# Optimization experiments

Hardware: AMD Instinct MI355X
Metric: run time of the kernel (lower is better)

## Reference

```python
import jax, jax.numpy as jnp
import numpy as np

SPIKING_T = 8        # args['spiking_t']
V_TH = 1.0           # spikingjelly IFNode default v_threshold
TAU = 2.0            # NonSpikingLIFNode tau
ALPHA = 4.0          # spikingjelly default Sigmoid surrogate alpha
MIN_LOG_STD, MAX_LOG_STD = -20.0, 2.0
LOG_2PI = float(np.log(2.0 * np.pi))

@jax.custom_vjp
def spike(x):
    # Heaviside forward (spikingjelly surrogate.Sigmoid behavior)
    return (x >= 0.0).astype(x.dtype)

def _spike_fwd(x):
    return spike(x), x

def _spike_bwd(x, g):
    s = jax.nn.sigmoid(ALPHA * x)
    return (g * ALPHA * s * (1.0 - s),)

spike.defvjp(_spike_fwd, _spike_bwd)


def setup_inputs() -> dict:
    key = jax.random.key(0)
    ks = jax.random.split(key, 8)
    B, N, H, A = 8192, 128, 1024, 32
    def lin_w(k, fan_in, fan_out):
        return jax.random.normal(k, (fan_in, fan_out), dtype=jnp.float32) / jnp.sqrt(float(fan_in))
    return {
        "state": jax.random.normal(ks[0], (B, N), dtype=jnp.float32),
        "w1": lin_w(ks[1], N, H),
        "b1": jnp.full((H,), 1e-6, dtype=jnp.float32),
        "w2": lin_w(ks[2], H, H),
        "b2": jnp.full((H,), 1e-6, dtype=jnp.float32),
        "w3": lin_w(ks[3], H, 2 * A),
        "b3": jnp.full((2 * A,), 1e-6, dtype=jnp.float32),
        "eps": jax.random.normal(ks[4], (B, A), dtype=jnp.float32),
    }


def reference(state, w1, b1, w2, b2, w3, b3, eps):
    B = state.shape[0]
    H = w1.shape[1]
    O = w3.shape[1]
    v1 = jnp.zeros((B, H), state.dtype)
    v2 = jnp.zeros((B, H), state.dtype)
    v3 = jnp.zeros((B, O), state.dtype)

    def step(carry, _):
        v1, v2, v3 = carry
        # IF node 1: charge, fire, hard reset to 0
        h1 = v1 + state @ w1 + b1
        s1 = spike(h1 - V_TH)
        v1 = h1 * (1.0 - s1)
        # IF node 2
        h2 = v2 + s1 @ w2 + b2
        s2 = spike(h2 - V_TH)
        v2 = h2 * (1.0 - s2)
        # NonSpiking LIF (decay_input=True, v_reset=0): v += (x - v)/tau
        x3 = s2 @ w3 + b3
        v3 = v3 + (x3 - v3) / TAU
        return (v1, v2, v3), None

    (v1, v2, v3), _ = jax.lax.scan(step, (v1, v2, v3), None, length=SPIKING_T)

    mu, log_std = jnp.split(v3, 2, axis=-1)
    log_std = jnp.clip(log_std, MIN_LOG_STD, MAX_LOG_STD)
    std = jnp.exp(log_std)
    z = mu + std * eps            # Normal rsample
    action = jnp.tanh(z)
    # Normal(mu, std).log_prob(z) = -eps^2/2 - log_std - 0.5*log(2*pi)
    log_prob = (-0.5 * eps * eps - log_std - 0.5 * LOG_2PI) \
               - jnp.log(1.0 - action * action + 1e-7)
    log_prob = jnp.sum(log_prob, axis=-1, keepdims=True)
    return action, log_prob
```

## Files before the change

kernel.cpp:

```cpp
#include <hip/hip_runtime.h>

typedef float    f32x4 __attribute__((ext_vector_type(4)));
typedef int      i32x4 __attribute__((ext_vector_type(4)));
typedef unsigned u32x4 __attribute__((ext_vector_type(4)));

typedef const __attribute__((address_space(1))) void* gptr_t;
typedef __attribute__((address_space(3))) void* lptr_t;

__device__ __forceinline__ void gload_lds16(const void* g, void* l) {
  __builtin_amdgcn_global_load_lds((gptr_t)g, (lptr_t)l, 16, 0, 0);
}

constexpr int Bsz  = 8192;
constexpr int Nin  = 128;
constexpr int Hd   = 1024;
constexpr int Aact = 32;
constexpr int Od   = 64;
constexpr int KC = 384;
constexpr float DELTA = 1.5e-4f;
constexpr unsigned WCAP = 262144;

constexpr float CSCALE = 1.1920928955078125e-7f;

__global__ __launch_bounds__(256)
void prep_kernel(const float* __restrict__ state, const float* __restrict__ w1,
                 const float* __restrict__ b1,
                 const float* __restrict__ w2, const float* __restrict__ w3,
                 unsigned char* __restrict__ s1pack,
                 char* __restrict__ p1, char* __restrict__ p2, char* __restrict__ p3,
                 char* __restrict__ r1, char* __restrict__ r2, char* __restrict__ r3,
                 float* __restrict__ w2tf, unsigned* __restrict__ wcnt) {
  __shared__ float sAT[64][68];
  __shared__ float sB[64][68];
  const int tid = threadIdx.x;

  if (blockIdx.x >= 2048) {
    if (blockIdx.x == 2048 && tid < 8) wcnt[tid] = 0;
    const int u = (blockIdx.x - 2048) * 4 + (tid >> 6);
    const int lane = tid & 63;
    const int l15 = lane & 15, quad = lane >> 4;
    const int pn = u >> 4;
    const int kb = u & 15;
    const bool isw3 = (pn >= Hd / 16);
    const int pnl = isw3 ? pn - Hd / 16 : pn;
    const float* src = isw3 ? w3 : w2;
    const int N = isw3 ? Od : Hd;
    const int n = pnl * 16 + l15;
    const int k0 = kb * 64 + quad * 16;
    char* d1 = isw3 ? r1 : p1;
    char* d2 = isw3 ? r2 : p2;
    char* d3 = isw3 ? r3 : p3;
    float wv[16];
    char o1[16], o2[16], o3[16];
#pragma unroll
    for (int e = 0; e < 16; ++e) {
      float w = src[(size_t)(k0 + e) * N + n];
      wv[e] = w;
      float m1 = rintf(w * 512.0f);
      float q1 = w - m1 * (1.0f / 512.0f);
      float m2 = rintf(q1 * 65536.0f);
      float q2 = q1 - m2 * (1.0f / 65536.0f);
      float m3 = rintf(q2 * 8388608.0f);
      o1[e] = (char)(int)m1; o2[e] = (char)(int)m2; o3[e] = (char)(int)m3;
    }
    size_t off = ((size_t)pnl * 16 + kb) * 1024 + (size_t)lane * 16;
#pragma unroll
    for (int e = 0; e < 16; ++e) {
      d1[off + e] = o1[e]; d2[off + e] = o2[e]; d3[off + e] = o3[e];
    }
    if (!isw3) {
#pragma unroll
      for (int e = 0; e < 16; ++e)
        w2tf[(size_t)n * Hd + k0 + e] = wv[e];
    }
    return;
  }

  const int m0 = (blockIdx.x & 127) * 64, n0 = (blockIdx.x >> 7) * 64;
  const int tx = tid & 15, ty = tid >> 4;
  float acc[4][4] = {};
#pragma unroll
  for (int h = 0; h < 2; ++h) {
    if (h) __syncthreads();
    for (int idx = tid; idx < 1024; idx += 256) {
      int r = idx >> 4, c4 = (idx & 15) << 2;
      float4 v = *(const float4*)(state + (size_t)(m0 + r) * Nin + h * 64 + c4);
      int pc = (r + c4) & 63;
      sAT[c4 + 0][pc] = v.x; sAT[c4 + 1][pc] = v.y;
      sAT[c4 + 2][pc] = v.z; sAT[c4 + 3][pc] = v.w;
    }
    for (int idx = tid; idx < 1024; idx += 256) {
      int r = idx >> 4, c4 = (idx & 15) << 2;
      *(float4*)&sB[r][c4] = *(const float4*)(w1 + (size_t)(h * 64 + r) * Hd + n0 + c4);
    }
    __syncthreads();
    for (int k = 0; k < 64; ++k) {
      int cb = ((ty << 2) + (k & ~3)) & 63;
      float4 a4 = *(const float4*)&sAT[k][cb];
      float4 b = *(const float4*)&sB[k][tx * 4];
      float a[4] = {a4.x, a4.y, a4.z, a4.w};
#pragma unroll
      for (int i = 0; i < 4; ++i) {
        acc[i][0] = __fmaf_rn(a[i], b.x, acc[i][0]);
        acc[i][1] = __fmaf_rn(a[i], b.y, acc[i][1]);
        acc[i][2] = __fmaf_rn(a[i], b.z, acc[i][2]);
        acc[i][3] = __fmaf_rn(a[i], b.w, acc[i][3]);
      }
    }
  }
#pragma unroll
  for (int i = 0; i < 4; ++i) {
    int m = m0 + ty * 4 + i;
    unsigned pack = 0;
#pragma unroll
    for (int j = 0; j < 4; ++j) {
      int n = n0 + tx * 4 + j;
      float x = acc[i][j];
      float bb = b1[n];
      float v = 0.0f;
      unsigned bits = 0;
#pragma unroll
      for (int t = 0; t < 8; ++t) {
        float h2 = __fadd_rn(__fadd_rn(v, x), bb);
        if (h2 >= 1.0f) { bits |= (1u << t); v = 0.0f; } else { v = h2; }
      }
      pack |= bits << (8 * j);
    }
    *(unsigned*)(s1pack + (size_t)m * Hd + n0 + tx * 4) = pack;
  }
}

__global__ __launch_bounds__(256, 3)
void gemm2i8_kernel(const unsigned char* __restrict__ s1pack,
                    const char* __restrict__ q1, const char* __restrict__ q2,
                    const char* __restrict__ q3,
                    const float* __restrict__ b2,
                    unsigned char* __restrict__ s2p,
                    unsigned* __restrict__ wcnt, unsigned* __restrict__ wlist) {
  constexpr int NKB = Hd / 64;
  __shared__ __align__(16) unsigned char lA[3][64 * 64];
  __shared__ __align__(16) char lB[3][3072];
  const int tid = threadIdx.x;
  const int m0 = blockIdx.x * 64;
  const int n0 = blockIdx.y * 16;
  const int wave = tid >> 6, lane = tid & 63, l15 = lane & 15, quad = lane >> 4;
  const char* bplane = (wave == 0) ? q1 : (wave == 1) ? q2 : q3;
  const unsigned char* asrc = s1pack
      + (size_t)(m0 + ((tid >> 6) << 4) + (tid & 15)) * Hd + ((tid >> 4) & 3) * 16;
  const char* bsrc2 = bplane + (size_t)blockIdx.y * NKB * 1024 + (size_t)lane * 16;
  i32x4 acc[3][8] = {};

  auto stage = [&](int kb, int buf) {
    gload_lds16(asrc + kb * 64, &lA[buf][tid * 16]);
    if (wave < 3)
      gload_lds16(bsrc2 + (size_t)kb * 1024, &lB[buf][wave * 1024 + lane * 16]);
  };
  stage(0, 0); stage(1, 1);

#pragma unroll
  for (int kb = 0; kb < NKB; ++kb) {
    const int cur = kb % 3;
    if (kb < NKB - 1) {
      if (wave < 3) asm volatile("s_waitcnt vmcnt(2)" ::: "memory");
      else          asm volatile("s_waitcnt vmcnt(1)" ::: "memory");
    } else {
      asm volatile("s_waitcnt vmcnt(0)" ::: "memory");
    }
    __builtin_amdgcn_s_barrier();
    asm volatile("" ::: "memory");
    u32x4 ad = *(const u32x4*)&lA[cur][wave * 1024 + lane * 16];
    i32x4 fb0 = *(const i32x4*)&lB[cur][lane * 16];
    i32x4 fb1 = *(const i32x4*)&lB[cur][1024 + lane * 16];
    i32x4 fb2 = *(const i32x4*)&lB[cur][2048 + lane * 16];
    if (kb + 2 < NKB) stage(kb + 2, (kb + 2) % 3);
#pragma unroll
    for (int t = 0; t < 8; ++t) {
      const unsigned msk = 0x01010101u << t;
      i32x4 af;
      af[0] = (int)(ad[0] & msk);
      af[1] = (int)(ad[1] & msk);
      af[2] = (int)(ad[2] & msk);
      af[3] = (int)(ad[3] & msk);
      acc[0][t] = __builtin_amdgcn_mfma_i32_16x16x64_i8(af, fb0, acc[0][t], 0, 0, 0);
      acc[1][t] = __builtin_amdgcn_mfma_i32_16x16x64_i8(af, fb1, acc[1][t], 0, 0, 0);
      acc[2][t] = __builtin_amdgcn_mfma_i32_16x16x64_i8(af, fb2, acc[2][t], 0, 0, 0);
    }
  }
  const int n = n0 + l15;
  const float bb = b2[n];
#pragma unroll
  for (int r = 0; r < 4; ++r) {
    int m = m0 + wave * 16 + quad * 4 + r;
    size_t idx = (size_t)m * Hd + n;
    float v = 0.0f;
    unsigned bits = 0;
#pragma unroll
    for (int t = 0; t < 8; ++t) {
      int a0 = acc[0][t][r] >> t;
      int a1 = acc[1][t][r] >> t;
      int a2 = acc[2][t][r] >> t;
      int s = (a0 << 14) + (a1 << 7) + a2;
      float G = (float)s * ((t == 7) ? -CSCALE : CSCALE);
      float h = __fadd_rn(__fadd_rn(v, G), bb);
      if (__builtin_expect(__builtin_fabsf(h - 1.0f) < DELTA, 0)) {
        unsigned pos = atomicAdd(wcnt, 1u);
        if (pos < WCAP) wlist[pos] = (unsigned)idx;
      }
      bool sp = (h >= 1.0f);
      if (sp) bits |= (1u << t);
      v = sp ? 0.0f : h;
    }
    s2p[idx] = (unsigned char)bits;
  }
}

__global__ __launch_bounds__(256)
void fixup_kernel(const unsigned* __restrict__ wcnt, const unsigned* __restrict__ wlist,
                  const unsigned char* __restrict__ s1pack, const float* __restrict__ w2tf,
                  const float* __restrict__ b2, unsigned char* __restrict__ s2p) {
  unsigned cnt = *wcnt;
  if (cnt > WCAP) cnt = WCAP;
  const int tid = threadIdx.x;
  const int lane = tid & 63;
  const int sl = lane / 3, blk3 = lane - sl * 3;
  const int wid = blockIdx.x * (blockDim.x >> 6) + (tid >> 6);
  const int nwaves = gridDim.x * (blockDim.x >> 6);
  for (unsigned base = (unsigned)wid * 21u; base < cnt; base += (unsigned)nwaves * 21u) {
    unsigned site = base + (unsigned)sl;
    bool act = (sl < 21) && (site < cnt);
    unsigned idx = act ? wlist[site] : 0u;
    int m = (int)(idx >> 10), n = (int)(idx & 1023u);
    const unsigned char* prow = s1pack + ((size_t)m << 10);
    const float* col = w2tf + ((size_t)n << 10);
    int kb = blk3 * KC;
    int kend = (blk3 == 2) ? Hd : kb + KC;
    float S[8] = {};
    if (act) {
      for (int k = kb; k < kend; k += 8) {
        float4 wa = *(const float4*)(col + k);
        float4 wb = *(const float4*)(col + k + 4);
        unsigned b0 = *(const unsigned*)(prow + k);
        unsigned b1 = *(const unsigned*)(prow + k + 4);
#pragma unroll
        for (int tau = 0; tau < 8; ++tau) {
          S[tau] = __fadd_rn(S[tau], ((b0 >> tau) & 1)        ? wa.x : 0.0f);
          S[tau] = __fadd_rn(S[tau], ((b0 >> (8 + tau)) & 1)  ? wa.y : 0.0f);
          S[tau] = __fadd_rn(S[tau], ((b0 >> (16 + tau)) & 1) ? wa.z : 0.0f);
          S[tau] = __fadd_rn(S[tau], ((b0 >> (24 + tau)) & 1) ? wa.w : 0.0f);
          S[tau] = __fadd_rn(S[tau], ((b1 >> tau) & 1)        ? wb.x : 0.0f);
          S[tau] = __fadd_rn(S[tau], ((b1 >> (8 + tau)) & 1)  ? wb.y : 0.0f);
          S[tau] = __fadd_rn(S[tau], ((b1 >> (16 + tau)) & 1) ? wb.z : 0.0f);
          S[tau] = __fadd_rn(S[tau], ((b1 >> (24 + tau)) & 1) ? wb.w : 0.0f);
        }
      }
    }
    float G[8];
#pragma unroll
    for (int tau = 0; tau < 8; ++tau) {
      float sB = __shfl(S[tau], lane + 1);
      float sC = __shfl(S[tau], lane + 2);
      G[tau] = __fadd_rn(__fadd_rn(S[tau], sB), sC);
    }
    if (act && blk3 == 0) {
      float bb = b2[n];
      float v = 0.0f;
      unsigned bits = 0;
      for (int tau = 0; tau < 8; ++tau) {
        float h = __fadd_rn(__fadd_rn(v, G[tau]), bb);
        bool sp = (h >= 1.0f);
        if (sp) bits |= (1u << tau);
        v = sp ? 0.0f : h;
      }
      s2p[idx] = (unsigned char)bits;
    }
  }
}

__global__ __launch_bounds__(256, 3)
void gemm3f_kernel(const unsigned char* __restrict__ s2p,
                   const char* __restrict__ q1, const char* __restrict__ q2,
                   const char* __restrict__ q3,
                   const float* __restrict__ b3, const float* __restrict__ eps,
                   float* __restrict__ action, float* __restrict__ logp) {
  constexpr int NKB = Hd / 64;
  __shared__ float sv[16][65];
  const int tid = threadIdx.x;
  const int m0 = blockIdx.x * 16;
  const int wave = tid >> 6, lane = tid & 63, l15 = lane & 15, quad = lane >> 4;
  const unsigned char* asrc = s2p + (size_t)(m0 + l15) * Hd + (lane >> 4) * 16;
  const size_t boff = (size_t)wave * NKB * 1024 + (size_t)lane * 16;
  const char* bp0 = q1 + boff;
  const char* bp1 = q2 + boff;
  const char* bp2 = q3 + boff;
  i32x4 acc[3][8] = {};

  u32x4 a_cur = *(const u32x4*)asrc;
  i32x4 f0c = *(const i32x4*)bp0;
  i32x4 f1c = *(const i32x4*)bp1;
  i32x4 f2c = *(const i32x4*)bp2;
#pragma unroll
  for (int kb = 0; kb < NKB; ++kb) {
    u32x4 a_nxt = a_cur; i32x4 f0n = f0c, f1n = f1c, f2n = f2c;
    if (kb + 1 < NKB) {
      a_nxt = *(const u32x4*)(asrc + (kb + 1) * 64);
      f0n = *(const i32x4*)(bp0 + (size_t)(kb + 1) * 1024);
      f1n = *(const i32x4*)(bp1 + (size_t)(kb + 1) * 1024);
      f2n = *(const i32x4*)(bp2 + (size_t)(kb + 1) * 1024);
    }
#pragma unroll
    for (int t = 0; t < 8; ++t) {
      const unsigned msk = 0x01010101u << t;
      i32x4 af;
      af[0] = (int)(a_cur[0] & msk);
      af[1] = (int)(a_cur[1] & msk);
      af[2] = (int)(a_cur[2] & msk);
      af[3] = (int)(a_cur[3] & msk);
      acc[0][t] = __builtin_amdgcn_mfma_i32_16x16x64_i8(af, f0c, acc[0][t], 0, 0, 0);
      acc[1][t] = __builtin_amdgcn_mfma_i32_16x16x64_i8(af, f1c, acc[1][t], 0, 0, 0);
      acc[2][t] = __builtin_amdgcn_mfma_i32_16x16x64_i8(af, f2c, acc[2][t], 0, 0, 0);
    }
    a_cur = a_nxt; f0c = f0n; f1c = f1n; f2c = f2n;
  }
  const int n = wave * 16 + l15;
  const float bb = b3[n];
#pragma unroll
  for (int r = 0; r < 4; ++r) {
    int row = quad * 4 + r;
    float v = 0.0f;
#pragma unroll
    for (int t = 0; t < 8; ++t) {
      int a0 = acc[0][t][r] >> t;
      int a1 = acc[1][t][r] >> t;
      int a2 = acc[2][t][r] >> t;
      int s = (a0 << 14) + (a1 << 7) + a2;
      float ge = (float)s * ((t == 7) ? -CSCALE : CSCALE);
      float x3 = __fadd_rn(ge, bb);
      float dd = __fsub_rn(x3, v);
      v = __fadd_rn(v, __fmul_rn(dd, 0.5f));
    }
    sv[row][n] = v;
  }
  __syncthreads();
#pragma unroll
  for (int pass = 0; pass < 2; ++pass) {
    int row = (pass << 3) + (tid >> 5);
    int j = tid & 31;
    float mu = sv[row][j];
    float ls = sv[row][32 + j];
    ls = fminf(fmaxf(ls, -20.0f), 2.0f);
    float sd = (float)exp((double)ls);
    float e  = eps[(size_t)(m0 + row) * Aact + j];
    float z  = __fadd_rn(mu, __fmul_rn(sd, e));
    float a;
    if (__builtin_fabsf(z) >= 7.90531111f) a = __builtin_copysignf(1.0f, z);
    else                                   a = (float)tanh((double)z);
    float aa = __fmul_rn(a, a);
    float u  = __fadd_rn(__fsub_rn(1.0f, aa), 1e-7f);
    float lg = (float)log((double)u);
    float l  = __fmul_rn(__fmul_rn(-0.5f, e), e);
    l = __fsub_rn(l, ls);
    l = __fsub_rn(l, 0.9189385332046727f);
    float term = __fsub_rn(l, lg);
    action[(size_t)(m0 + row) * Aact + j] = a;
    double lp = (double)term;
#pragma unroll
    for (int w = 16; w >= 1; w >>= 1) lp += __shfl_xor(lp, w);
    if (j == 0) logp[m0 + row] = (float)lp;
  }
}

extern "C" void kernel_launch(void* const* d_in, const int* in_sizes, int n_in,
                              void* d_out, int out_size, void* d_ws, size_t ws_size,
                              hipStream_t stream) {
  const float* state = (const float*)d_in[0];
  const float* w1 = (const float*)d_in[1];
  const float* b1 = (const float*)d_in[2];
  const float* w2 = (const float*)d_in[3];
  const float* b2 = (const float*)d_in[4];
  const float* w3 = (const float*)d_in[5];
  const float* b3 = (const float*)d_in[6];
  const float* eps = (const float*)d_in[7];
  float* out_action = (float*)d_out;
  float* out_logp = out_action + (size_t)Bsz * Aact;

  char* p = (char*)d_ws;
  auto take = [&](size_t bytes) {
    char* r = p;
    p += (bytes + 255) & ~(size_t)255;
    return r;
  };
  unsigned char* s1pack = (unsigned char*)take((size_t)Bsz * Hd);
  unsigned char* s2p = (unsigned char*)take((size_t)Bsz * Hd);
  char* w2q1 = (char*)take((size_t)Hd * Hd);
  char* w2q2 = (char*)take((size_t)Hd * Hd);
  char* w2q3 = (char*)take((size_t)Hd * Hd);
  char* w3q1 = (char*)take((size_t)Hd * Od);
  char* w3q2 = (char*)take((size_t)Hd * Od);
  char* w3q3 = (char*)take((size_t)Hd * Od);
  float* w2tf = (float*)take((size_t)Hd * Hd * 4);
  unsigned* wcnt = (unsigned*)take(8 * 4);
  unsigned* wlist = (unsigned*)take((size_t)WCAP * 4);

  prep_kernel<<<2048 + 272, 256, 0, stream>>>(state, w1, b1, w2, w3, s1pack,
                                              w2q1, w2q2, w2q3, w3q1, w3q2, w3q3,
                                              w2tf, wcnt);
  gemm2i8_kernel<<<dim3(Bsz / 64, Hd / 16), 256, 0, stream>>>(s1pack, w2q1, w2q2, w2q3,
                                                              b2, s2p, wcnt, wlist);
  fixup_kernel<<<256, 256, 0, stream>>>(wcnt, wlist, s1pack, w2tf, b2, s2p);

  gemm3f_kernel<<<Bsz / 16, 256, 0, stream>>>(s2p, w3q1, w3q2, w3q3, b3, eps,
                                              out_action, out_logp);
}
```

Before: 287.4 us.

## Split gemm2 timesteps across twice as many waves and reduce via LDS

```diff
diff --git a/kernel.cpp b/kernel.cpp
--- a/kernel.cpp
+++ b/kernel.cpp
@@ -130,7 +130,7 @@
   }
 }
 
-__global__ __launch_bounds__(256, 3)
+__global__ __launch_bounds__(512, 4)
 void gemm2i8_kernel(const unsigned char* __restrict__ s1pack,
                     const char* __restrict__ q1, const char* __restrict__ q2,
                     const char* __restrict__ q3,
@@ -140,20 +140,27 @@
   constexpr int NKB = Hd / 64;
   __shared__ __align__(16) unsigned char lA[3][64 * 64];
   __shared__ __align__(16) char lB[3][3072];
+  __shared__ float sG[64][145];
   const int tid = threadIdx.x;
   const int m0 = blockIdx.x * 64;
   const int n0 = blockIdx.y * 16;
   const int wave = tid >> 6, lane = tid & 63, l15 = lane & 15, quad = lane >> 4;
-  const char* bplane = (wave == 0) ? q1 : (wave == 1) ? q2 : q3;
+  const int wrow = wave & 3;
+  const int wt4 = (wave >> 2) << 2;
   const unsigned char* asrc = s1pack
       + (size_t)(m0 + ((tid >> 6) << 4) + (tid & 15)) * Hd + ((tid >> 4) & 3) * 16;
+  const char* bplane = (wave == 4) ? q1 : (wave == 5) ? q2 : q3;
   const char* bsrc2 = bplane + (size_t)blockIdx.y * NKB * 1024 + (size_t)lane * 16;
-  i32x4 acc[3][8] = {};
+  i32x4 acc[3][4] = {};
+  unsigned msk[4];
+#pragma unroll
+  for (int tt = 0; tt < 4; ++tt) msk[tt] = 0x01010101u << (wt4 + tt);
 
   auto stage = [&](int kb, int buf) {
-    gload_lds16(asrc + kb * 64, &lA[buf][tid * 16]);
-    if (wave < 3)
-      gload_lds16(bsrc2 + (size_t)kb * 1024, &lB[buf][wave * 1024 + lane * 16]);
+    if (wave < 4)
+      gload_lds16(asrc + kb * 64, &lA[buf][tid * 16]);
+    else if (wave < 7)
+      gload_lds16(bsrc2 + (size_t)kb * 1024, &lB[buf][(wave - 4) * 1024 + lane * 16]);
   };
   stage(0, 0); stage(1, 1);
 
@@ -161,47 +168,55 @@
   for (int kb = 0; kb < NKB; ++kb) {
     const int cur = kb % 3;
     if (kb < NKB - 1) {
-      if (wave < 3) asm volatile("s_waitcnt vmcnt(2)" ::: "memory");
-      else          asm volatile("s_waitcnt vmcnt(1)" ::: "memory");
+      asm volatile("s_waitcnt vmcnt(1)" ::: "memory");
     } else {
       asm volatile("s_waitcnt vmcnt(0)" ::: "memory");
     }
     __builtin_amdgcn_s_barrier();
     asm volatile("" ::: "memory");
-    u32x4 ad = *(const u32x4*)&lA[cur][wave * 1024 + lane * 16];
+    u32x4 ad = *(const u32x4*)&lA[cur][wrow * 1024 + lane * 16];
     i32x4 fb0 = *(const i32x4*)&lB[cur][lane * 16];
     i32x4 fb1 = *(const i32x4*)&lB[cur][1024 + lane * 16];
     i32x4 fb2 = *(const i32x4*)&lB[cur][2048 + lane * 16];
     if (kb + 2 < NKB) stage(kb + 2, (kb + 2) % 3);
 #pragma unroll
-    for (int t = 0; t < 8; ++t) {
-      const unsigned msk = 0x01010101u << t;
+    for (int tt = 0; tt < 4; ++tt) {
       i32x4 af;
-      af[0] = (int)(ad[0] & msk);
-      af[1] = (int)(ad[1] & msk);
-      af[2] = (int)(ad[2] & msk);
-      af[3] = (int)(ad[3] & msk);
-      acc[0][t] = __builtin_amdgcn_mfma_i32_16x16x64_i8(af, fb0, acc[0][t], 0, 0, 0);
-      acc[1][t] = __builtin_amdgcn_mfma_i32_16x16x64_i8(af, fb1, acc[1][t], 0, 0, 0);
-      acc[2][t] = __builtin_amdgcn_mfma_i32_16x16x64_i8(af, fb2, acc[2][t], 0, 0, 0);
-    }
-  }
-  const int n = n0 + l15;
-  const float bb = b2[n];
+      af[0] = (int)(ad[0] & msk[tt]);
+      af[1] = (int)(ad[1] & msk[tt]);
+      af[2] = (int)(ad[2] & msk[tt]);
+      af[3] = (int)(ad[3] & msk[tt]);
+      acc[0][tt] = __builtin_amdgcn_mfma_i32_16x16x64_i8(af, fb0, acc[0][tt], 0, 0, 0);
+      acc[1][tt] = __builtin_amdgcn_mfma_i32_16x16x64_i8(af, fb1, acc[1][tt], 0, 0, 0);
+      acc[2][tt] = __builtin_amdgcn_mfma_i32_16x16x64_i8(af, fb2, acc[2][tt], 0, 0, 0);
+    }
+  }
 #pragma unroll
   for (int r = 0; r < 4; ++r) {
-    int m = m0 + wave * 16 + quad * 4 + r;
-    size_t idx = (size_t)m * Hd + n;
+    int row = wrow * 16 + quad * 4 + r;
+#pragma unroll
+    for (int tt = 0; tt < 4; ++tt) {
+      int t = wt4 + tt;
+      int a0 = acc[0][tt][r] >> t;
+      int a1 = acc[1][tt][r] >> t;
+      int a2 = acc[2][tt][r] >> t;
+      int s = (a0 << 14) + (a1 << 7) + a2;
+      sG[row][l15 * 9 + t] = (float)s * ((t == 7) ? -CSCALE : CSCALE);
+    }
+  }
+  __syncthreads();
+#pragma unroll
+  for (int ss = 0; ss < 2; ++ss) {
+    int site = tid + ss * 512;
+    int row = site >> 4, col = site & 15;
+    const float* Gp = &sG[row][col * 9];
+    float bb = b2[n0 + col];
+    size_t idx = (size_t)(m0 + row) * Hd + (n0 + col);
     float v = 0.0f;
     unsigned bits = 0;
 #pragma unroll
     for (int t = 0; t < 8; ++t) {
-      int a0 = acc[0][t][r] >> t;
-      int a1 = acc[1][t][r] >> t;
-      int a2 = acc[2][t][r] >> t;
-      int s = (a0 << 14) + (a1 << 7) + a2;
-      float G = (float)s * ((t == 7) ? -CSCALE : CSCALE);
-      float h = __fadd_rn(__fadd_rn(v, G), bb);
+      float h = __fadd_rn(__fadd_rn(v, Gp[t]), bb);
       if (__builtin_expect(__builtin_fabsf(h - 1.0f) < DELTA, 0)) {
         unsigned pos = atomicAdd(wcnt, 1u);
         if (pos < WCAP) wlist[pos] = (unsigned)idx;
@@ -404,7 +419,7 @@
   prep_kernel<<<2048 + 272, 256, 0, stream>>>(state, w1, b1, w2, w3, s1pack,
                                               w2q1, w2q2, w2q3, w3q1, w3q2, w3q3,
                                               w2tf, wcnt);
-  gemm2i8_kernel<<<dim3(Bsz / 64, Hd / 16), 256, 0, stream>>>(s1pack, w2q1, w2q2, w2q3,
+  gemm2i8_kernel<<<dim3(Bsz / 64, Hd / 16), 512, 0, stream>>>(s1pack, w2q1, w2q2, w2q3,
                                                               b2, s2p, wcnt, wlist);
   fixup_kernel<<<256, 256, 0, stream>>>(wcnt, wlist, s1pack, w2tf, b2, s2p);
 
```

New measurement: 318.9 us. +11.0%, slower.
